# Kernel optimization log

Measured on AMD Instinct MI355X. Metric: run time of the kernel, lower is better.

## Reference

```python
import jax, jax.numpy as jnp
import numpy as np

N, E, CIN, COUT, KHOP = 100000, 600000, 128, 128, 3


def setup_inputs() -> dict:
    key = jax.random.key(0)
    k1, k2, k3 = jax.random.split(key, 3)
    x = jax.random.normal(k1, (N, CIN), dtype=jnp.float32)
    edge_index = jax.random.randint(k2, (2, E), 0, N, dtype=jnp.int64)
    # xavier_uniform init for weight [in, out]
    limit = float(np.sqrt(6.0 / (CIN + COUT)))
    weight = jax.random.uniform(k3, (CIN, COUT), minval=-limit, maxval=limit, dtype=jnp.float32)
    bias = jnp.zeros((COUT,), jnp.float32)
    log_scale = jnp.asarray(np.log(1.0), jnp.float32)  # init_scale = 1.0
    hop_logits = jnp.zeros((KHOP + 1,), jnp.float32)
    return {"x": x, "edge_index": edge_index, "num_nodes": N,
            "weight": weight, "bias": bias,
            "log_scale": log_scale, "hop_logits": hop_logits}


def reference(x, edge_index, num_nodes, weight, bias, log_scale, hop_logits):
    src, dst = edge_index[0], edge_index[1]
    # symmetric normalization D_src^{-1/2} A D_dst^{-1/2}, no self-loops
    ones = jnp.ones(src.shape, x.dtype)
    deg_src = jax.ops.segment_sum(ones, src, num_segments=num_nodes)
    deg_dst = jax.ops.segment_sum(ones, dst, num_segments=num_nodes)
    dsi = jnp.where(deg_src > 0, jax.lax.rsqrt(jnp.maximum(deg_src, 1.0)), 0.0)
    ddi = jnp.where(deg_dst > 0, jax.lax.rsqrt(jnp.maximum(deg_dst, 1.0)), 0.0)
    edge_weight = dsi[src] * ddi[dst]  # [E]

    s = jnp.exp(log_scale)
    alpha = jax.nn.softmax(hop_logits)  # [k_hop+1]

    wavelet_out = alpha[0] * x
    current = x
    for k in range(1, KHOP + 1):  # small fixed hop count
        # A_hat @ current : gather -> scale -> scatter-add
        current = jax.ops.segment_sum(current[src] * edge_weight[:, None], dst,
                                      num_segments=num_nodes)
        decay = jnp.exp(-s * k)
        wavelet_out = wavelet_out + alpha[k] * decay * current

    return wavelet_out @ weight + bias
```

## Files before the change

kernel.cpp:

```cpp
#include <hip/hip_runtime.h>
#include <hip/hip_bf16.h>

#define C 128
#define WELL 32

typedef short s16x8 __attribute__((ext_vector_type(8)));
typedef float f32x4 __attribute__((ext_vector_type(4)));

static __device__ __forceinline__ float b2f(unsigned short u) {
    union { unsigned int i; float f; } v;
    v.i = ((unsigned int)u) << 16;
    return v.f;
}
static __device__ __forceinline__ unsigned short f2b(float f) {
    __hip_bfloat16 b = __float2bfloat16(f);
    return *reinterpret_cast<unsigned short*>(&b);
}

__global__ __launch_bounds__(256) void zero_int_kernel(int4* __restrict__ p, long n4) {
    long i = blockIdx.x * 256L + threadIdx.x;
    if (i < n4) p[i] = make_int4(0, 0, 0, 0);
}

__global__ __launch_bounds__(256) void hist_kernel(
    const int* __restrict__ ei, int E,
    int* __restrict__ degs, int* __restrict__ degd) {
    int i = blockIdx.x * 256 + threadIdx.x;
    int e0 = i * 4;
    if (e0 + 4 <= E) {
        int4 s = *(const int4*)(ei + e0);
        int4 d = *(const int4*)(ei + E + e0);
        atomicAdd(&degs[s.x], 1); atomicAdd(&degs[s.y], 1);
        atomicAdd(&degs[s.z], 1); atomicAdd(&degs[s.w], 1);
        atomicAdd(&degd[d.x], 1); atomicAdd(&degd[d.y], 1);
        atomicAdd(&degd[d.z], 1); atomicAdd(&degd[d.w], 1);
    } else {
        for (int e = e0; e < E; ++e) {
            atomicAdd(&degs[ei[e]], 1);
            atomicAdd(&degd[ei[E + e]], 1);
        }
    }
}

__global__ __launch_bounds__(256) void wt_kernel(const float* __restrict__ W,
                                                 unsigned short* __restrict__ WtB,
                                                 const float* __restrict__ log_scale,
                                                 const float* __restrict__ hop_logits,
                                                 float* __restrict__ coef) {
    int tid = blockIdx.x * 256 + threadIdx.x;
    int k = tid & 127, c = tid >> 7;
    WtB[c * 128 + k] = f2b(W[k * 128 + c]);
    if (tid == 0) {
        float s = expf(log_scale[0]);
        float m = hop_logits[0];
        for (int kk = 1; kk < 4; ++kk) m = fmaxf(m, hop_logits[kk]);
        float a[4], sum = 0.0f;
        for (int kk = 0; kk < 4; ++kk) { a[kk] = expf(hop_logits[kk] - m); sum += a[kk]; }
        for (int kk = 0; kk < 4; ++kk) coef[kk] = (a[kk] / sum) * expf(-s * (float)kk);
    }
}

__global__ __launch_bounds__(256) void scatter_kernel(const int* __restrict__ ei, int E,
                                                      int* __restrict__ cursor,
                                                      const int* __restrict__ degs,
                                                      int2* __restrict__ ell) {
    int i = blockIdx.x * 256 + threadIdx.x;
    int e0 = i * 4;
    if (e0 + 4 <= E) {
        int4 s = *(const int4*)(ei + e0);
        int4 d = *(const int4*)(ei + E + e0);
        float w0 = rsqrtf((float)degs[s.x]);
        float w1 = rsqrtf((float)degs[s.y]);
        float w2 = rsqrtf((float)degs[s.z]);
        float w3 = rsqrtf((float)degs[s.w]);
        int p0 = atomicAdd(&cursor[d.x], 1);
        int p1 = atomicAdd(&cursor[d.y], 1);
        int p2 = atomicAdd(&cursor[d.z], 1);
        int p3 = atomicAdd(&cursor[d.w], 1);
        if (p0 < WELL) ell[(long)d.x * WELL + p0] = make_int2(s.x, __float_as_int(w0));
        if (p1 < WELL) ell[(long)d.y * WELL + p1] = make_int2(s.y, __float_as_int(w1));
        if (p2 < WELL) ell[(long)d.z * WELL + p2] = make_int2(s.z, __float_as_int(w2));
        if (p3 < WELL) ell[(long)d.w * WELL + p3] = make_int2(s.w, __float_as_int(w3));
    } else {
        for (int e = e0; e < E; ++e) {
            int s = ei[e];
            int d = ei[E + e];
            float w = rsqrtf((float)degs[s]);
            int pos = atomicAdd(&cursor[d], 1);
            if (pos < WELL) ell[(long)d * WELL + pos] = make_int2(s, __float_as_int(w));
        }
    }
}

template<int SRCF32>
__global__ __launch_bounds__(256) void pull_kernel(
    const int2* __restrict__ ell, const int* __restrict__ degd,
    const void* __restrict__ cur, unsigned int* __restrict__ nxt, int N) {
    int wid = (int)((blockIdx.x * 256L + threadIdx.x) >> 6);
    if (wid >= N) return;
    int lane = threadIdx.x & 63;
    int cnt = __builtin_amdgcn_readfirstlane(degd[wid]);
    cnt = cnt < WELL ? cnt : WELL;
    long base = (long)wid * WELL;
    const float2* curf = (const float2*)cur;
    const unsigned int* curb = (const unsigned int*)cur;
    float sx = 0.f, sy = 0.f;
    if (cnt > 0) {
        for (int j = 0; j < cnt; j += 8) {
            int   idx[8];
            float wt[8];
            #pragma unroll
            for (int i = 0; i < 8; ++i) {
                int jj = j + i;
                bool ok = jj < cnt;
                int2 e = ell[base + (ok ? jj : 0)];
                idx[i] = e.x;
                wt[i] = ok ? __int_as_float(e.y) : 0.0f;
            }
            if (SRCF32) {
                float2 v[8];
                #pragma unroll
                for (int i = 0; i < 8; ++i) v[i] = curf[(long)idx[i] * 64 + lane];
                #pragma unroll
                for (int i = 0; i < 8; ++i) { sx += wt[i] * v[i].x; sy += wt[i] * v[i].y; }
            } else {
                unsigned int u[8];
                #pragma unroll
                for (int i = 0; i < 8; ++i) u[i] = curb[(long)idx[i] * 64 + lane];
                #pragma unroll
                for (int i = 0; i < 8; ++i) {
                    sx += wt[i] * b2f((unsigned short)(u[i] & 0xffff));
                    sy += wt[i] * b2f((unsigned short)(u[i] >> 16));
                }
            }
        }
        float dv = rsqrtf((float)cnt);
        sx *= dv; sy *= dv;
    }
    unsigned int o = (unsigned int)f2b(sx) | ((unsigned int)f2b(sy) << 16);
    nxt[(long)wid * 64 + lane] = o;
}

__global__ __launch_bounds__(256) void mfma_matmul_kernel(
    const float* __restrict__ x,
    const unsigned short* __restrict__ h1,
    const unsigned short* __restrict__ h2,
    const unsigned short* __restrict__ h3,
    const float* __restrict__ coef,
    const unsigned short* __restrict__ WtB,
    const float* __restrict__ bias,
    float* __restrict__ out, int N) {
    __shared__ unsigned short Wl[128 * 136];
    int t = threadIdx.x;

    #pragma unroll
    for (int i = 0; i < 8; ++i) {
        int ch = t + i * 256;
        int r = ch >> 4;
        int ko = (ch & 15) * 8;
        *(s16x8*)(Wl + r * 136 + ko) = *(const s16x8*)(WtB + r * 128 + ko);
    }
    float c0 = coef[0], c1 = coef[1], c2 = coef[2], c3 = coef[3];
    __syncthreads();

    int wave = t >> 6, lane = t & 63;
    int lsel = lane & 15;
    int lk   = (lane >> 4) * 8;
    int arow = blockIdx.x * 64 + wave * 16 + lsel;
    bool rok = arow < N;
    long rbase = (long)arow * C;

    f32x4 acc[8];
    #pragma unroll
    for (int i = 0; i < 8; ++i) acc[i] = (f32x4){0.f, 0.f, 0.f, 0.f};

    #pragma unroll
    for (int ks = 0; ks < 4; ++ks) {
        int k0 = ks * 32 + lk;
        s16x8 a;
        if (rok) {
            const float* xp = x + rbase + k0;
            float4 xa = *(const float4*)xp;
            float4 xb = *(const float4*)(xp + 4);
            s16x8 u1 = *(const s16x8*)(h1 + rbase + k0);
            s16x8 u2 = *(const s16x8*)(h2 + rbase + k0);
            s16x8 u3 = *(const s16x8*)(h3 + rbase + k0);
            float f0 = c0 * xa.x + c1 * b2f((unsigned short)u1[0]) + c2 * b2f((unsigned short)u2[0]) + c3 * b2f((unsigned short)u3[0]);
            float f1 = c0 * xa.y + c1 * b2f((unsigned short)u1[1]) + c2 * b2f((unsigned short)u2[1]) + c3 * b2f((unsigned short)u3[1]);
            float f2 = c0 * xa.z + c1 * b2f((unsigned short)u1[2]) + c2 * b2f((unsigned short)u2[2]) + c3 * b2f((unsigned short)u3[2]);
            float f3 = c0 * xa.w + c1 * b2f((unsigned short)u1[3]) + c2 * b2f((unsigned short)u2[3]) + c3 * b2f((unsigned short)u3[3]);
            float f4 = c0 * xb.x + c1 * b2f((unsigned short)u1[4]) + c2 * b2f((unsigned short)u2[4]) + c3 * b2f((unsigned short)u3[4]);
            float f5 = c0 * xb.y + c1 * b2f((unsigned short)u1[5]) + c2 * b2f((unsigned short)u2[5]) + c3 * b2f((unsigned short)u3[5]);
            float f6 = c0 * xb.z + c1 * b2f((unsigned short)u1[6]) + c2 * b2f((unsigned short)u2[6]) + c3 * b2f((unsigned short)u3[6]);
            float f7 = c0 * xb.w + c1 * b2f((unsigned short)u1[7]) + c2 * b2f((unsigned short)u2[7]) + c3 * b2f((unsigned short)u3[7]);
            a[0] = (short)f2b(f0); a[1] = (short)f2b(f1);
            a[2] = (short)f2b(f2); a[3] = (short)f2b(f3);
            a[4] = (short)f2b(f4); a[5] = (short)f2b(f5);
            a[6] = (short)f2b(f6); a[7] = (short)f2b(f7);
        } else {
            a = (s16x8)0;
        }
        #pragma unroll
        for (int cf = 0; cf < 8; ++cf) {
            s16x8 b = *(const s16x8*)(Wl + (cf * 16 + lsel) * 136 + k0);
            acc[cf] = __builtin_amdgcn_mfma_f32_16x16x32_bf16(a, b, acc[cf], 0, 0, 0);
        }
    }

    int orow0 = blockIdx.x * 64 + wave * 16 + (lane >> 4) * 4;
    #pragma unroll
    for (int cf = 0; cf < 8; ++cf) {
        int ocol = cf * 16 + lsel;
        float bv = bias[ocol];
        #pragma unroll
        for (int r = 0; r < 4; ++r) {
            int orow = orow0 + r;
            if (orow < N) out[(long)orow * C + ocol] = acc[cf][r] + bv;
        }
    }
}

extern "C" void kernel_launch(void* const* d_in, const int* in_sizes, int n_in,
                              void* d_out, int out_size, void* d_ws, size_t ws_size,
                              hipStream_t stream) {
    const float* x          = (const float*)d_in[0];
    const int*   ei         = (const int*)d_in[1];
    const float* W          = (const float*)d_in[3];
    const float* bias       = (const float*)d_in[4];
    const float* log_scale  = (const float*)d_in[5];
    const float* hop_logits = (const float*)d_in[6];
    float* out = (float*)d_out;

    int N = in_sizes[0] / C;
    int E = in_sizes[1] / 2;

    char* ws = (char*)d_ws;
    size_t hb = (size_t)N * C * sizeof(unsigned short);
    unsigned short* h1 = (unsigned short*)ws;
    unsigned short* h2 = (unsigned short*)(ws + hb);
    unsigned short* h3 = (unsigned short*)(ws + 2 * hb);
    int2*  ell     = (int2*)(ws + 3 * hb);
    int*   degs    = (int*)(ell + (long)N * WELL);
    int*   degd    = degs + N;
    int*   cursor  = degd + N;
    float* coef    = (float*)(cursor + N);
    unsigned short* WtB = (unsigned short*)(coef + 4);

    int eb4 = (E / 4 + 255) / 256 + 1;
    int pull_blocks = (int)(((long)N * 64 + 255) / 256);

    zero_int_kernel<<<(int)((3L * N / 4 + 255) / 256), 256, 0, stream>>>((int4*)degs, 3L * N / 4);
    hist_kernel<<<eb4, 256, 0, stream>>>(ei, E, degs, degd);
    wt_kernel<<<64, 256, 0, stream>>>(W, WtB, log_scale, hop_logits, coef);
    scatter_kernel<<<eb4, 256, 0, stream>>>(ei, E, cursor, degs, ell);

    pull_kernel<1><<<pull_blocks, 256, 0, stream>>>(ell, degd, x,  (unsigned int*)h1, N);
    pull_kernel<0><<<pull_blocks, 256, 0, stream>>>(ell, degd, h1, (unsigned int*)h2, N);
    pull_kernel<0><<<pull_blocks, 256, 0, stream>>>(ell, degd, h2, (unsigned int*)h3, N);

    mfma_matmul_kernel<<<(N + 63) / 64, 256, 0, stream>>>(x, h1, h2, h3, coef, WtB, bias, out, N);
}
```

Measured before the change: 262.8 us.

## Replace padded ELL with compact CSR and fuse hop combine into last pull

Drops the fixed-width 32-slot ELL adjacency in favour of a compact CSR built from a block-level prefix scan that uses an atomic global counter. The pull kernels now split each wave across several edges at once: two edges with float4 loads for the fp32 first hop, four edges with 16-byte bf16 loads for later hops, followed by cross-lane shuffle reductions. The last hop writes the coefficient-weighted combination of x, h1, h2 and h3 straight to a single bf16 buffer, so the GEMM reads one input instead of four. This cuts ELL memory traffic, removes the silent truncation of degrees above 32, and trims GEMM input bandwidth, at the cost of an extra scan kernel, shuffle reductions, and CSR row order that depends on atomic block ordering.

```diff
diff --git a/kernel.cpp b/kernel.cpp
--- a/kernel.cpp
+++ b/kernel.cpp
@@ -2,7 +2,6 @@
 #include <hip/hip_bf16.h>
 
 #define C 128
-#define WELL 32
 
 typedef short s16x8 __attribute__((ext_vector_type(8)));
 typedef float f32x4 __attribute__((ext_vector_type(4)));
@@ -60,10 +59,36 @@
     }
 }
 
+__global__ __launch_bounds__(256) void rpscan_kernel(const int* __restrict__ degd,
+                                                     int* __restrict__ rp,
+                                                     int* __restrict__ cursor,
+                                                     int* __restrict__ gctr, int N) {
+    __shared__ int sm[256];
+    __shared__ int base_sm;
+    int t = threadIdx.x;
+    int i = blockIdx.x * 256 + t;
+    int v = (i < N) ? degd[i] : 0;
+    sm[t] = v;
+    __syncthreads();
+    for (int off = 1; off < 256; off <<= 1) {
+        int add = (t >= off) ? sm[t - off] : 0;
+        __syncthreads();
+        sm[t] += add;
+        __syncthreads();
+    }
+    if (t == 255) base_sm = atomicAdd(gctr, sm[255]);
+    __syncthreads();
+    if (i < N) {
+        int r = base_sm + sm[t] - v;
+        rp[i] = r;
+        cursor[i] = r;
+    }
+}
+
 __global__ __launch_bounds__(256) void scatter_kernel(const int* __restrict__ ei, int E,
                                                       int* __restrict__ cursor,
                                                       const int* __restrict__ degs,
-                                                      int2* __restrict__ ell) {
+                                                      int2* __restrict__ csr) {
     int i = blockIdx.x * 256 + threadIdx.x;
     int e0 = i * 4;
     if (e0 + 4 <= E) {
@@ -77,76 +102,135 @@
         int p1 = atomicAdd(&cursor[d.y], 1);
         int p2 = atomicAdd(&cursor[d.z], 1);
         int p3 = atomicAdd(&cursor[d.w], 1);
-        if (p0 < WELL) ell[(long)d.x * WELL + p0] = make_int2(s.x, __float_as_int(w0));
-        if (p1 < WELL) ell[(long)d.y * WELL + p1] = make_int2(s.y, __float_as_int(w1));
-        if (p2 < WELL) ell[(long)d.z * WELL + p2] = make_int2(s.z, __float_as_int(w2));
-        if (p3 < WELL) ell[(long)d.w * WELL + p3] = make_int2(s.w, __float_as_int(w3));
+        csr[p0] = make_int2(s.x, __float_as_int(w0));
+        csr[p1] = make_int2(s.y, __float_as_int(w1));
+        csr[p2] = make_int2(s.z, __float_as_int(w2));
+        csr[p3] = make_int2(s.w, __float_as_int(w3));
     } else {
         for (int e = e0; e < E; ++e) {
             int s = ei[e];
             int d = ei[E + e];
             float w = rsqrtf((float)degs[s]);
             int pos = atomicAdd(&cursor[d], 1);
-            if (pos < WELL) ell[(long)d * WELL + pos] = make_int2(s, __float_as_int(w));
-        }
-    }
-}
-
-template<int SRCF32>
-__global__ __launch_bounds__(256) void pull_kernel(
-    const int2* __restrict__ ell, const int* __restrict__ degd,
-    const void* __restrict__ cur, unsigned int* __restrict__ nxt, int N) {
+            csr[pos] = make_int2(s, __float_as_int(w));
+        }
+    }
+}
+
+__global__ __launch_bounds__(256) void pull1_kernel(
+    const int* __restrict__ rp, const int* __restrict__ degd,
+    const int2* __restrict__ csr,
+    const float* __restrict__ x, unsigned int* __restrict__ nxt, int N) {
     int wid = (int)((blockIdx.x * 256L + threadIdx.x) >> 6);
     if (wid >= N) return;
     int lane = threadIdx.x & 63;
+    int g  = lane >> 5;
+    int ls = lane & 31;
+    int beg = __builtin_amdgcn_readfirstlane(rp[wid]);
     int cnt = __builtin_amdgcn_readfirstlane(degd[wid]);
-    cnt = cnt < WELL ? cnt : WELL;
-    long base = (long)wid * WELL;
-    const float2* curf = (const float2*)cur;
-    const unsigned int* curb = (const unsigned int*)cur;
-    float sx = 0.f, sy = 0.f;
+    float a0 = 0.f, a1 = 0.f, a2 = 0.f, a3 = 0.f;
     if (cnt > 0) {
         for (int j = 0; j < cnt; j += 8) {
-            int   idx[8];
-            float wt[8];
             #pragma unroll
-            for (int i = 0; i < 8; ++i) {
-                int jj = j + i;
+            for (int h = 0; h < 4; ++h) {
+                int jj = j + 2 * h + g;
                 bool ok = jj < cnt;
-                int2 e = ell[base + (ok ? jj : 0)];
-                idx[i] = e.x;
-                wt[i] = ok ? __int_as_float(e.y) : 0.0f;
+                int2 e = csr[beg + (ok ? jj : 0)];
+                float w = ok ? __int_as_float(e.y) : 0.0f;
+                float4 v = *(const float4*)(x + (long)e.x * C + ls * 4);
+                a0 += w * v.x; a1 += w * v.y; a2 += w * v.z; a3 += w * v.w;
             }
-            if (SRCF32) {
-                float2 v[8];
-                #pragma unroll
-                for (int i = 0; i < 8; ++i) v[i] = curf[(long)idx[i] * 64 + lane];
-                #pragma unroll
-                for (int i = 0; i < 8; ++i) { sx += wt[i] * v[i].x; sy += wt[i] * v[i].y; }
-            } else {
-                unsigned int u[8];
-                #pragma unroll
-                for (int i = 0; i < 8; ++i) u[i] = curb[(long)idx[i] * 64 + lane];
-                #pragma unroll
-                for (int i = 0; i < 8; ++i) {
-                    sx += wt[i] * b2f((unsigned short)(u[i] & 0xffff));
-                    sy += wt[i] * b2f((unsigned short)(u[i] >> 16));
-                }
-            }
-        }
+        }
+        a0 += __shfl_xor(a0, 32, 64);
+        a1 += __shfl_xor(a1, 32, 64);
+        a2 += __shfl_xor(a2, 32, 64);
+        a3 += __shfl_xor(a3, 32, 64);
         float dv = rsqrtf((float)cnt);
-        sx *= dv; sy *= dv;
-    }
-    unsigned int o = (unsigned int)f2b(sx) | ((unsigned int)f2b(sy) << 16);
-    nxt[(long)wid * 64 + lane] = o;
-}
-
-__global__ __launch_bounds__(256) void mfma_matmul_kernel(
+        a0 *= dv; a1 *= dv; a2 *= dv; a3 *= dv;
+    }
+    if (g == 0) {
+        uint2 o;
+        o.x = (unsigned int)f2b(a0) | ((unsigned int)f2b(a1) << 16);
+        o.y = (unsigned int)f2b(a2) | ((unsigned int)f2b(a3) << 16);
+        *(uint2*)((unsigned short*)nxt + (long)wid * C + ls * 4) = o;
+    }
+}
+
+template<int COMBINE>
+__global__ __launch_bounds__(256) void pullb_kernel(
+    const int* __restrict__ rp, const int* __restrict__ degd,
+    const int2* __restrict__ csr,
+    const unsigned short* __restrict__ cur,
+    unsigned short* __restrict__ nxt,
     const float* __restrict__ x,
     const unsigned short* __restrict__ h1,
-    const unsigned short* __restrict__ h2,
-    const unsigned short* __restrict__ h3,
-    const float* __restrict__ coef,
+    const float* __restrict__ coef, int N) {
+    int wid = (int)((blockIdx.x * 256L + threadIdx.x) >> 6);
+    if (wid >= N) return;
+    int lane = threadIdx.x & 63;
+    int g  = lane >> 4;
+    int ls = lane & 15;
+    int beg = __builtin_amdgcn_readfirstlane(rp[wid]);
+    int cnt = __builtin_amdgcn_readfirstlane(degd[wid]);
+    float acc[8] = {0.f, 0.f, 0.f, 0.f, 0.f, 0.f, 0.f, 0.f};
+    if (cnt > 0) {
+        for (int j = 0; j < cnt; j += 8) {
+            int2 e0, e1; float w0, w1;
+            {
+                int jj = j + g;
+                bool ok = jj < cnt;
+                e0 = csr[beg + (ok ? jj : 0)];
+                w0 = ok ? __int_as_float(e0.y) : 0.0f;
+            }
+            {
+                int jj = j + 4 + g;
+                bool ok = jj < cnt;
+                e1 = csr[beg + (ok ? jj : 0)];
+                w1 = ok ? __int_as_float(e1.y) : 0.0f;
+            }
+            s16x8 u0 = *(const s16x8*)(cur + (long)e0.x * C + ls * 8);
+            s16x8 u1 = *(const s16x8*)(cur + (long)e1.x * C + ls * 8);
+            #pragma unroll
+            for (int k = 0; k < 8; ++k)
+                acc[k] += w0 * b2f((unsigned short)u0[k]) + w1 * b2f((unsigned short)u1[k]);
+        }
+        #pragma unroll
+        for (int k = 0; k < 8; ++k) acc[k] += __shfl_xor(acc[k], 16, 64);
+        #pragma unroll
+        for (int k = 0; k < 8; ++k) acc[k] += __shfl_xor(acc[k], 32, 64);
+        float dv = rsqrtf((float)cnt);
+        #pragma unroll
+        for (int k = 0; k < 8; ++k) acc[k] *= dv;
+    }
+    if (g == 0) {
+        long rb = (long)wid * C + ls * 8;
+        float f[8];
+        if (COMBINE) {
+            float c0 = coef[0], c1 = coef[1], c2 = coef[2], c3 = coef[3];
+            float4 xa = *(const float4*)(x + rb);
+            float4 xb = *(const float4*)(x + rb + 4);
+            s16x8 u1 = *(const s16x8*)(h1 + rb);
+            s16x8 u2 = *(const s16x8*)(cur + rb);
+            float xv[8] = {xa.x, xa.y, xa.z, xa.w, xb.x, xb.y, xb.z, xb.w};
+            #pragma unroll
+            for (int k = 0; k < 8; ++k)
+                f[k] = c0 * xv[k] + c1 * b2f((unsigned short)u1[k])
+                     + c2 * b2f((unsigned short)u2[k]) + c3 * acc[k];
+        } else {
+            #pragma unroll
+            for (int k = 0; k < 8; ++k) f[k] = acc[k];
+        }
+        uint4 o;
+        o.x = (unsigned int)f2b(f[0]) | ((unsigned int)f2b(f[1]) << 16);
+        o.y = (unsigned int)f2b(f[2]) | ((unsigned int)f2b(f[3]) << 16);
+        o.z = (unsigned int)f2b(f[4]) | ((unsigned int)f2b(f[5]) << 16);
+        o.w = (unsigned int)f2b(f[6]) | ((unsigned int)f2b(f[7]) << 16);
+        *(uint4*)(nxt + rb) = o;
+    }
+}
+
+__global__ __launch_bounds__(256) void gemm_kernel(
+    const unsigned short* __restrict__ hc,
     const unsigned short* __restrict__ WtB,
     const float* __restrict__ bias,
     float* __restrict__ out, int N) {
@@ -160,7 +244,6 @@
         int ko = (ch & 15) * 8;
         *(s16x8*)(Wl + r * 136 + ko) = *(const s16x8*)(WtB + r * 128 + ko);
     }
-    float c0 = coef[0], c1 = coef[1], c2 = coef[2], c3 = coef[3];
     __syncthreads();
 
     int wave = t >> 6, lane = t & 63;
@@ -177,29 +260,7 @@
     #pragma unroll
     for (int ks = 0; ks < 4; ++ks) {
         int k0 = ks * 32 + lk;
-        s16x8 a;
-        if (rok) {
-            const float* xp = x + rbase + k0;
-            float4 xa = *(const float4*)xp;
-            float4 xb = *(const float4*)(xp + 4);
-            s16x8 u1 = *(const s16x8*)(h1 + rbase + k0);
-            s16x8 u2 = *(const s16x8*)(h2 + rbase + k0);
-            s16x8 u3 = *(const s16x8*)(h3 + rbase + k0);
-            float f0 = c0 * xa.x + c1 * b2f((unsigned short)u1[0]) + c2 * b2f((unsigned short)u2[0]) + c3 * b2f((unsigned short)u3[0]);
-            float f1 = c0 * xa.y + c1 * b2f((unsigned short)u1[1]) + c2 * b2f((unsigned short)u2[1]) + c3 * b2f((unsigned short)u3[1]);
-            float f2 = c0 * xa.z + c1 * b2f((unsigned short)u1[2]) + c2 * b2f((unsigned short)u2[2]) + c3 * b2f((unsigned short)u3[2]);
-            float f3 = c0 * xa.w + c1 * b2f((unsigned short)u1[3]) + c2 * b2f((unsigned short)u2[3]) + c3 * b2f((unsigned short)u3[3]);
-            float f4 = c0 * xb.x + c1 * b2f((unsigned short)u1[4]) + c2 * b2f((unsigned short)u2[4]) + c3 * b2f((unsigned short)u3[4]);
-            float f5 = c0 * xb.y + c1 * b2f((unsigned short)u1[5]) + c2 * b2f((unsigned short)u2[5]) + c3 * b2f((unsigned short)u3[5]);
-            float f6 = c0 * xb.z + c1 * b2f((unsigned short)u1[6]) + c2 * b2f((unsigned short)u2[6]) + c3 * b2f((unsigned short)u3[6]);
-            float f7 = c0 * xb.w + c1 * b2f((unsigned short)u1[7]) + c2 * b2f((unsigned short)u2[7]) + c3 * b2f((unsigned short)u3[7]);
-            a[0] = (short)f2b(f0); a[1] = (short)f2b(f1);
-            a[2] = (short)f2b(f2); a[3] = (short)f2b(f3);
-            a[4] = (short)f2b(f4); a[5] = (short)f2b(f5);
-            a[6] = (short)f2b(f6); a[7] = (short)f2b(f7);
-        } else {
-            a = (s16x8)0;
-        }
+        s16x8 a = rok ? *(const s16x8*)(hc + rbase + k0) : (s16x8)0;
         #pragma unroll
         for (int cf = 0; cf < 8; ++cf) {
             s16x8 b = *(const s16x8*)(Wl + (cf * 16 + lsel) * 136 + k0);
@@ -238,25 +299,30 @@
     size_t hb = (size_t)N * C * sizeof(unsigned short);
     unsigned short* h1 = (unsigned short*)ws;
     unsigned short* h2 = (unsigned short*)(ws + hb);
-    unsigned short* h3 = (unsigned short*)(ws + 2 * hb);
-    int2*  ell     = (int2*)(ws + 3 * hb);
-    int*   degs    = (int*)(ell + (long)N * WELL);
+    unsigned short* hc = (unsigned short*)(ws + 2 * hb);
+    int2*  csr     = (int2*)(ws + 3 * hb);
+    int*   degs    = (int*)(csr + E);
     int*   degd    = degs + N;
-    int*   cursor  = degd + N;
+    int*   gctr    = degd + N;
+    int*   rp      = gctr + 16;
+    int*   cursor  = rp + N;
     float* coef    = (float*)(cursor + N);
     unsigned short* WtB = (unsigned short*)(coef + 4);
 
     int eb4 = (E / 4 + 255) / 256 + 1;
+    int nbk = (N + 255) / 256;
     int pull_blocks = (int)(((long)N * 64 + 255) / 256);
 
-    zero_int_kernel<<<(int)((3L * N / 4 + 255) / 256), 256, 0, stream>>>((int4*)degs, 3L * N / 4);
+    long zn4 = (2L * N + 16 + 3) / 4;
+    zero_int_kernel<<<(int)((zn4 + 255) / 256), 256, 0, stream>>>((int4*)degs, zn4);
     hist_kernel<<<eb4, 256, 0, stream>>>(ei, E, degs, degd);
     wt_kernel<<<64, 256, 0, stream>>>(W, WtB, log_scale, hop_logits, coef);
-    scatter_kernel<<<eb4, 256, 0, stream>>>(ei, E, cursor, degs, ell);
-
-    pull_kernel<1><<<pull_blocks, 256, 0, stream>>>(ell, degd, x,  (unsigned int*)h1, N);
-    pull_kernel<0><<<pull_blocks, 256, 0, stream>>>(ell, degd, h1, (unsigned int*)h2, N);
-    pull_kernel<0><<<pull_blocks, 256, 0, stream>>>(ell, degd, h2, (unsigned int*)h3, N);
-
-    mfma_matmul_kernel<<<(N + 63) / 64, 256, 0, stream>>>(x, h1, h2, h3, coef, WtB, bias, out, N);
-}
+    rpscan_kernel<<<nbk, 256, 0, stream>>>(degd, rp, cursor, gctr, N);
+    scatter_kernel<<<eb4, 256, 0, stream>>>(ei, E, cursor, degs, csr);
+
+    pull1_kernel<<<pull_blocks, 256, 0, stream>>>(rp, degd, csr, x, (unsigned int*)h1, N);
+    pullb_kernel<0><<<pull_blocks, 256, 0, stream>>>(rp, degd, csr, h1, h2, x, h1, coef, N);
+    pullb_kernel<1><<<pull_blocks, 256, 0, stream>>>(rp, degd, csr, h2, hc, x, h1, coef, N);
+
+    gemm_kernel<<<(N + 63) / 64, 256, 0, stream>>>(hc, WtB, bias, out, N);
+}
```

Measured after the change: 251.2 us. -4.4%, faster.
